# Kernel tuning notes

Hardware: AMD Instinct MI355X
Metric: run time of the kernel (lower is better)

The kernel has to match this reference:

```python
import jax, jax.numpy as jnp
import numpy as np

D_MODEL = 1024
N_HEADS = 16
HEAD_DIM = D_MODEL // N_HEADS


def setup_inputs() -> dict:
    key = jax.random.key(0)
    ks = jax.random.split(key, 9)
    B, S, D = 2, 2048, D_MODEL
    scale = 1.0 / np.sqrt(D)
    return {
        "q": jax.random.normal(ks[0], (B, S, D), jnp.float32),
        "k": jax.random.normal(ks[1], (B, S, D), jnp.float32),
        "v": jax.random.normal(ks[2], (B, S, D), jnp.float32),
        "Wq": jax.random.normal(ks[3], (D, D), jnp.float32) * scale,
        "bq": jax.random.normal(ks[4], (D,), jnp.float32) * 0.01,
        "Wk": jax.random.normal(ks[5], (D, D), jnp.float32) * scale,
        "bk": jax.random.normal(ks[6], (D,), jnp.float32) * 0.01,
        "Wv": jax.random.normal(ks[7], (D, D), jnp.float32) * scale,
        "bv": jax.random.normal(ks[8], (D,), jnp.float32) * 0.01,
    }


def reference(q, k, v, Wq, bq, Wk, bk, Wv, bv):
    B, S, D = q.shape
    H, Dh = N_HEADS, D // N_HEADS
    # linear projections (torch Linear: x @ W.T + b)
    qp = q @ Wq.T + bq
    kp = k @ Wk.T + bk
    vp = v @ Wv.T + bv
    # [B, S, H, Dh] -> [B, H, S, Dh]
    qh = qp.reshape(B, S, H, Dh).transpose(0, 2, 1, 3)
    kh = kp.reshape(B, S, H, Dh).transpose(0, 2, 1, 3)
    vh = vp.reshape(B, S, H, Dh).transpose(0, 2, 1, 3)
    # scaled dot-product attention (mask=None path)
    scores = jnp.einsum('bhqd,bhkd->bhqk', qh, kh) / jnp.sqrt(jnp.asarray(Dh, qh.dtype))
    attn = jax.nn.softmax(scores, axis=-1)
    out = jnp.einsum('bhqk,bhkd->bhqd', attn, vh)
    # [B, H, S, Dh] -> [B, S, D]
    return out.transpose(0, 2, 1, 3).reshape(B, S, D)
```

## Files before the change

kernel.cpp:

```cpp
#include <hip/hip_runtime.h>
#include <stdint.h>
#include <stddef.h>


#define NH  16
#define DH  64
#define SEQ 2048
#define DM  1024
#define NB  2

#define ACT_N (NB * SEQ * DM)
#define W_N   (DM * DM)
#define QSCALE 0.18033688011116012f

typedef float  f32x4  __attribute__((ext_vector_type(4)));
typedef __bf16 bf16x8 __attribute__((ext_vector_type(8)));
typedef __bf16 bf16x4 __attribute__((ext_vector_type(4)));

__device__ __forceinline__ __bf16 f2bf(float f) { return (__bf16)f; }

__device__ __forceinline__ float fexp2(float x) {
    float r; asm("v_exp_f32 %0, %1" : "=v"(r) : "v"(x)); return r;
}

__device__ __forceinline__ void gload_lds16(const void* g, void* l) {
    __builtin_amdgcn_global_load_lds(
        (const __attribute__((address_space(1))) void*)g,
        (__attribute__((address_space(3))) void*)l, 16, 0, 0);
}

__global__ __launch_bounds__(256) void cvt6(
    const float* __restrict__ s0, const float* __restrict__ s1,
    const float* __restrict__ s2, const float* __restrict__ s3,
    const float* __restrict__ s4, const float* __restrict__ s5,
    __bf16* __restrict__ d0, __bf16* __restrict__ d1, __bf16* __restrict__ d2,
    __bf16* __restrict__ d3, __bf16* __restrict__ d4, __bf16* __restrict__ d5)
{
    const float* s; __bf16* d; int n;
    switch (blockIdx.z) {
        case 0: s = s0; d = d0; n = ACT_N; break;
        case 1: s = s1; d = d1; n = ACT_N; break;
        case 2: s = s2; d = d2; n = ACT_N; break;
        case 3: s = s3; d = d3; n = W_N;   break;
        case 4: s = s4; d = d4; n = W_N;   break;
        default: s = s5; d = d5; n = W_N;  break;
    }
    const size_t i = ((size_t)blockIdx.x * 256 + threadIdx.x) * 8;
    if (i >= (size_t)n) return;
    float4 f0 = *(const float4*)(s + i);
    float4 f1 = *(const float4*)(s + i + 4);
    bf16x8 o;
    o[0] = f2bf(f0.x); o[1] = f2bf(f0.y); o[2] = f2bf(f0.z); o[3] = f2bf(f0.w);
    o[4] = f2bf(f1.x); o[5] = f2bf(f1.y); o[6] = f2bf(f1.z); o[7] = f2bf(f1.w);
    *(bf16x8*)(d + i) = o;
}

__global__ __launch_bounds__(512) void proj3(
    const __bf16* __restrict__ Xq, const __bf16* __restrict__ Xk, const __bf16* __restrict__ Xv,
    const __bf16* __restrict__ Wq, const __bf16* __restrict__ Wk, const __bf16* __restrict__ Wv,
    const float* __restrict__ bq, const float* __restrict__ bk, const float* __restrict__ bv,
    __bf16* __restrict__ dq, __bf16* __restrict__ dk, __bf16* __restrict__ dv)
{
    __shared__ __align__(16) __bf16 sA[2][16384];
    __shared__ __align__(16) __bf16 sB[2][16384];

    const int tid  = threadIdx.x;
    const int lane = tid & 63;
    const int wv   = tid >> 6;
    const int wm   = wv >> 2;
    const int wn   = wv & 3;
    const int tensor = blockIdx.y >> 2;
    const int nb   = (blockIdx.y & 3) * 256;
    const int mb   = blockIdx.x * 256;

    const __bf16 *X, *W; const float* bias; __bf16* dst;
    if (tensor == 0)      { X = Xq; W = Wq; bias = bq; dst = dq; }
    else if (tensor == 1) { X = Xk; W = Wk; bias = bk; dst = dk; }
    else                  { X = Xv; W = Wv; bias = bv; dst = dv; }
    const bool vpath = (tensor == 2);

    const int lr = lane & 15;
    const int lg = lane >> 4;

    const int srow = lane >> 3;
    const int gch  = (lane & 7) ^ srow;
    const __bf16* xs = X + (size_t)(mb + wv * 32 + srow) * DM + gch * 8;
    const __bf16* ws = W + (size_t)(nb + wv * 32 + srow) * DM + gch * 8;

#define LA(BUF, T, I) gload_lds16(xs + (size_t)(T) * 64 + (size_t)(I) * 8 * DM, \
                                  &sA[BUF][(wv * 32 + (I) * 8) * 64])
#define LB(BUF, T, I) gload_lds16(ws + (size_t)(T) * 64 + (size_t)(I) * 8 * DM, \
                                  &sB[BUF][(wv * 32 + (I) * 8) * 64])

    const int rsw = (lr & 7) << 4;
    const int rdk0 = (0 * 64 + lg * 16) ^ rsw;
    const int rdk1 = (1 * 64 + lg * 16) ^ rsw;
    const int arow = (wm * 128 + lr) * 128;
    const int brow = (wn * 64 + lr) * 128;

    f32x4 acc[32];
#pragma unroll
    for (int i = 0; i < 32; ++i) acc[i] = (f32x4){0.f, 0.f, 0.f, 0.f};

    bf16x8 aP[4], aQ2[4], bP[4], bQ2[4];

#define RDA(R, CA, MH, KS) { \
    _Pragma("unroll") for (int mt = 0; mt < 4; ++mt) \
        R[mt] = *(const bf16x8*)((CA) + arow + ((MH) * 4 + mt) * 16 * 128 + ((KS) ? rdk1 : rdk0)); }
#define RDB(R, CB, KS) { \
    _Pragma("unroll") for (int nt = 0; nt < 4; ++nt) \
        R[nt] = *(const bf16x8*)((CB) + brow + nt * 16 * 128 + ((KS) ? rdk1 : rdk0)); }

#define MFMAQ(MH, AA, BB) { \
    __builtin_amdgcn_s_setprio(1); \
    if (!vpath) { \
        _Pragma("unroll") for (int nt = 0; nt < 4; ++nt) \
        _Pragma("unroll") for (int mt = 0; mt < 4; ++mt) \
            acc[nt * 8 + (MH) * 4 + mt] = __builtin_amdgcn_mfma_f32_16x16x32_bf16( \
                BB[nt], AA[mt], acc[nt * 8 + (MH) * 4 + mt], 0, 0, 0); \
    } else { \
        _Pragma("unroll") for (int mt = 0; mt < 4; ++mt) \
        _Pragma("unroll") for (int nt = 0; nt < 4; ++nt) \
            acc[((MH) * 4 + mt) * 4 + nt] = __builtin_amdgcn_mfma_f32_16x16x32_bf16( \
                AA[mt], BB[nt], acc[((MH) * 4 + mt) * 4 + nt], 0, 0, 0); } \
    __builtin_amdgcn_s_setprio(0); }

#pragma unroll
    for (int i = 0; i < 4; ++i) { LA(0, 0, i); LB(0, 0, i); }
    __syncthreads();
    {
        const char* ca = (const char*)&sA[0][0];
        const char* cb = (const char*)&sB[0][0];
        RDA(aP, ca, 0, 0);
        RDB(bP, cb, 0);
    }

#pragma unroll
    for (int t = 0; t < 16; ++t) {
        const int cur = t & 1, nxt = cur ^ 1;
        const char* ca = (const char*)&sA[cur][0];
        const char* cb = (const char*)&sB[cur][0];
        const char* caN = (const char*)&sA[nxt][0];
        const char* cbN = (const char*)&sB[nxt][0];
        const bool more = (t + 1 < 16);

        if (more) { LA(nxt, t + 1, 0); LA(nxt, t + 1, 1); LB(nxt, t + 1, 0); }
        RDA(aQ2, ca, 1, 0);
        MFMAQ(0, aP, bP);

        if (more) { LA(nxt, t + 1, 2); LA(nxt, t + 1, 3); LB(nxt, t + 1, 1); }
        RDA(aP, ca, 0, 1);
        RDB(bQ2, cb, 1);
        MFMAQ(1, aQ2, bP);

        if (more) { LB(nxt, t + 1, 2); LB(nxt, t + 1, 3); }
        RDA(aQ2, ca, 1, 1);
        MFMAQ(0, aP, bQ2);

        MFMAQ(1, aQ2, bQ2);
        if (more) {
            __syncthreads();
            RDA(aP, caN, 0, 0);
            RDB(bP, cbN, 0);
        }
    }
#undef MFMAQ
#undef RDA
#undef RDB
#undef LA
#undef LB

    if (!vpath) {
        const float scale = (tensor == 0) ? QSCALE : 1.0f;
#pragma unroll
        for (int nt = 0; nt < 4; ++nt) {
            const int n_base = nb + wn * 64 + nt * 16 + lg * 4;
            const float4 bb = *(const float4*)&bias[n_base];
            const int h = n_base >> 6, dh = n_base & 63;
#pragma unroll
            for (int mt = 0; mt < 8; ++mt) {
                const int m_g = mb + wm * 128 + mt * 16 + lr;
                const int bi = m_g >> 11;
                const int s  = m_g & (SEQ - 1);
                const f32x4 v = acc[nt * 8 + mt];
                bf16x4 w;
                w[0] = f2bf((v[0] + bb.x) * scale);
                w[1] = f2bf((v[1] + bb.y) * scale);
                w[2] = f2bf((v[2] + bb.z) * scale);
                w[3] = f2bf((v[3] + bb.w) * scale);
                *(bf16x4*)&dst[((size_t)((bi * NH + h) * SEQ + s)) * DH + dh] = w;
            }
        }
    } else {
        const int h = (nb + wn * 64) >> 6;
#pragma unroll
        for (int nt = 0; nt < 4; ++nt) {
            const int n_g = nb + wn * 64 + nt * 16 + lr;
            const float bb = bias[n_g];
            const int dh = n_g & 63;
#pragma unroll
            for (int mt = 0; mt < 8; ++mt) {
                const int m_g = mb + wm * 128 + mt * 16 + lg * 4;
                const int bi = m_g >> 11;
                const int s0 = m_g & (SEQ - 1);
                const f32x4 v = acc[mt * 4 + nt];
                bf16x4 w;
#pragma unroll
                for (int r = 0; r < 4; ++r) w[r] = f2bf(v[r] + bb);
                *(bf16x4*)&dst[((size_t)((bi * NH + h) * DH + dh)) * SEQ + s0] = w;
            }
        }
    }
}

__global__ __launch_bounds__(256) void attn_kernel(
    const __bf16* __restrict__ qh, const __bf16* __restrict__ kh,
    const __bf16* __restrict__ vT, float* __restrict__ out)
{
    __shared__ __align__(16) __bf16 kbuf[3][4096];
    __shared__ __align__(16) __bf16 vbuf[3][4096];

    const int tid  = threadIdx.x;
    const int lane = tid & 63;
    const int wv   = tid >> 6;
    const int i    = blockIdx.x;
    const int slot = i >> 3;
    const int bh   = (i & 7) * 4 + (slot >> 4);
    const int qt   = slot & 15;
    const size_t hb = (size_t)bh * SEQ * DH;
    const int q0 = qt * 128 + wv * 32;
    const int lq = lane & 15;
    const int lg = lane >> 4;
    const int swz = (lq & 7) << 4;

    const int p0 = tid, p1 = tid + 256;
    const int c0 = (p0 ^ ((p0 >> 3) & 7)) & 7;
    const int c1 = (p1 ^ ((p1 >> 3) & 7)) & 7;
    const int r0 = p0 >> 3, r1 = p1 >> 3;
    const int gr0 = (r0 & 35) | ((r0 & 12) << 1) | ((r0 & 16) >> 2);
    const int gr1 = (r1 & 35) | ((r1 & 12) << 1) | ((r1 & 16) >> 2);
    const __bf16* ks0 = kh + hb + (size_t)gr0 * DH + c0 * 8;
    const __bf16* ks1 = kh + hb + (size_t)gr1 * DH + c1 * 8;
    const __bf16* vs0 = vT + hb + (size_t)r0 * SEQ + c0 * 8;
    const __bf16* vs1 = vT + hb + (size_t)r1 * SEQ + c1 * 8;
    const int dst0 = wv * 512;
    const int dst1 = 2048 + wv * 512;

#define STAGE(SEL, TI) { \
    gload_lds16(ks0 + (size_t)(TI) * 64 * DH, &kbuf[SEL][dst0]); \
    gload_lds16(ks1 + (size_t)(TI) * 64 * DH, &kbuf[SEL][dst1]); \
    gload_lds16(vs0 + (TI) * 64, &vbuf[SEL][dst0]); \
    gload_lds16(vs1 + (TI) * 64, &vbuf[SEL][dst1]); }

    bf16x8 bQ[2][2];
#pragma unroll
    for (int qtf = 0; qtf < 2; ++qtf)
#pragma unroll
        for (int ks = 0; ks < 2; ++ks)
            bQ[qtf][ks] = *(const bf16x8*)(qh + hb +
                (size_t)(q0 + qtf * 16 + lq) * DH + ks * 32 + lg * 8);

    bf16x8 ONES;
#pragma unroll
    for (int e = 0; e < 8; ++e) ONES[e] = f2bf(1.0f);

    f32x4 O[2][4];
#pragma unroll
    for (int qtf = 0; qtf < 2; ++qtf)
#pragma unroll
        for (int dt = 0; dt < 4; ++dt) O[qtf][dt] = (f32x4){0.f, 0.f, 0.f, 0.f};
    f32x4 Ol[2];
    Ol[0] = (f32x4){0.f, 0.f, 0.f, 0.f};
    Ol[1] = (f32x4){0.f, 0.f, 0.f, 0.f};

    const int rdk0 = lq * 128 + ((0 * 64 + lg * 16) ^ swz);
    const int rdk1 = lq * 128 + ((1 * 64 + lg * 16) ^ swz);

    f32x4 scA[2][4], scB[2][4];
    bf16x8 paf[2][2];

#define QK(SL, SC) { \
    const char* kc = (const char*)&kbuf[SL][0]; \
    _Pragma("unroll") for (int kt = 0; kt < 4; ++kt) { \
        const bf16x8 ak0 = *(const bf16x8*)(kc + kt * 2048 + rdk0); \
        const bf16x8 ak1 = *(const bf16x8*)(kc + kt * 2048 + rdk1); \
        _Pragma("unroll") for (int qtf = 0; qtf < 2; ++qtf) { \
            f32x4 c = (f32x4){0.f, 0.f, 0.f, 0.f}; \
            c = __builtin_amdgcn_mfma_f32_16x16x32_bf16(ak0, bQ[qtf][0], c, 0, 0, 0); \
            c = __builtin_amdgcn_mfma_f32_16x16x32_bf16(ak1, bQ[qtf][1], c, 0, 0, 0); \
            SC[qtf][kt] = c; } } }

#define SMAX(SC) { \
    _Pragma("unroll") for (int qtf = 0; qtf < 2; ++qtf) \
    _Pragma("unroll") for (int ks = 0; ks < 2; ++ks) { \
        bf16x8 w; \
        _Pragma("unroll") for (int r = 0; r < 4; ++r) { \
            w[r]     = f2bf(fexp2(SC[qtf][2 * ks][r])); \
            w[4 + r] = f2bf(fexp2(SC[qtf][2 * ks + 1][r])); } \
        paf[qtf][ks] = w; } }

#define PV(SL) { \
    const char* vc = (const char*)&vbuf[SL][0]; \
    _Pragma("unroll") for (int ks = 0; ks < 2; ++ks) { \
        const int rd = (ks == 0) ? rdk0 : rdk1; \
        _Pragma("unroll") for (int dt = 0; dt < 4; ++dt) { \
            const bf16x8 bv = *(const bf16x8*)(vc + dt * 2048 + rd); \
            O[0][dt] = __builtin_amdgcn_mfma_f32_16x16x32_bf16(paf[0][ks], bv, O[0][dt], 0, 0, 0); \
            O[1][dt] = __builtin_amdgcn_mfma_f32_16x16x32_bf16(paf[1][ks], bv, O[1][dt], 0, 0, 0); } \
        Ol[0] = __builtin_amdgcn_mfma_f32_16x16x32_bf16(paf[0][ks], ONES, Ol[0], 0, 0, 0); \
        Ol[1] = __builtin_amdgcn_mfma_f32_16x16x32_bf16(paf[1][ks], ONES, Ol[1], 0, 0, 0); } }

#define BODY(T, SCUR, SNXT) { \
    SMAX(SCUR); \
    __syncthreads(); \
    if ((T) + 2 < 32) STAGE(((T) + 2) % 3, (T) + 2); \
    __builtin_amdgcn_s_setprio(1); \
    if ((T) + 1 < 32) QK(((T) + 1) % 3, SNXT); \
    PV((T) % 3); \
    __builtin_amdgcn_s_setprio(0); }

    STAGE(0, 0);
    STAGE(1, 1);
    __syncthreads();
    QK(0, scA);

#pragma unroll
    for (int t = 0; t < 32; t += 2) {
        BODY(t, scA, scB);
        BODY(t + 1, scB, scA);
    }
#undef BODY
#undef PV
#undef SMAX
#undef QK
#undef STAGE

    const int b = bh >> 4, h = bh & 15;
#pragma unroll
    for (int qtf = 0; qtf < 2; ++qtf) {
#pragma unroll
        for (int r = 0; r < 4; ++r) {
            const float li = 1.0f / (qtf ? Ol[1][r] : Ol[0][r]);
            const int s_g = q0 + qtf * 16 + lg * 4 + r;
            float* op = out + ((size_t)(b * SEQ + s_g)) * DM + h * DH;
#pragma unroll
            for (int dt = 0; dt < 4; ++dt)
                op[dt * 16 + lq] = O[qtf][dt][r] * li;
        }
    }
}

extern "C" void kernel_launch(void* const* d_in, const int* in_sizes, int n_in,
                              void* d_out, int out_size, void* d_ws, size_t ws_size,
                              hipStream_t stream)
{
    (void)in_sizes; (void)n_in; (void)out_size; (void)ws_size;
    const float* q  = (const float*)d_in[0];
    const float* k  = (const float*)d_in[1];
    const float* v  = (const float*)d_in[2];
    const float* Wq = (const float*)d_in[3];
    const float* bq = (const float*)d_in[4];
    const float* Wk = (const float*)d_in[5];
    const float* bk = (const float*)d_in[6];
    const float* Wv = (const float*)d_in[7];
    const float* bv = (const float*)d_in[8];

    const size_t act = (size_t)ACT_N;
    const size_t wn  = (size_t)W_N;
    __bf16* qx  = (__bf16*)d_ws;
    __bf16* kx  = qx + act;
    __bf16* vx  = kx + act;
    __bf16* wqb = vx + act;
    __bf16* wkb = wqb + wn;
    __bf16* wvb = wkb + wn;
    __bf16* qhd = wvb + wn;
    __bf16* khd = qhd + act;
    __bf16* vhd = khd + act;
    float* out = (float*)d_out;

    cvt6<<<dim3(2048, 1, 6), dim3(256), 0, stream>>>(
        q, k, v, Wq, Wk, Wv, qx, kx, vx, wqb, wkb, wvb);
    proj3<<<dim3(16, 12), dim3(512), 0, stream>>>(
        qx, kx, vx, wqb, wkb, wvb, bq, bk, bv, qhd, khd, vhd);
    attn_kernel<<<dim3(512), dim3(256), 0, stream>>>(qhd, khd, vhd, out);
}
```

Measured before the change: 90.09 us.

## Shrink projection GEMM tiles to 128x128 with XCD-aware block remapping

The fused QKV projection now uses 128x128 output tiles computed by 256-thread blocks instead of 256x256 tiles with 512 threads, which raises the grid from 192 to 768 blocks so all compute units are filled. A linear block index is remapped so that consecutive tiles land on the same XCD group, aiming for better L2 reuse of X and W rows. Each warp's accumulators and the LDS footprint shrink, but every block gets less data reuse per tile and makes more global loads for the same work.

```diff
diff --git a/kernel.cpp b/kernel.cpp
--- a/kernel.cpp
+++ b/kernel.cpp
@@ -55,23 +55,21 @@
     *(bf16x8*)(d + i) = o;
 }
 
-__global__ __launch_bounds__(512) void proj3(
+__global__ __launch_bounds__(256) void proj3(
     const __bf16* __restrict__ Xq, const __bf16* __restrict__ Xk, const __bf16* __restrict__ Xv,
     const __bf16* __restrict__ Wq, const __bf16* __restrict__ Wk, const __bf16* __restrict__ Wv,
     const float* __restrict__ bq, const float* __restrict__ bk, const float* __restrict__ bv,
     __bf16* __restrict__ dq, __bf16* __restrict__ dk, __bf16* __restrict__ dv)
 {
-    __shared__ __align__(16) __bf16 sA[2][16384];
-    __shared__ __align__(16) __bf16 sB[2][16384];
-
-    const int tid  = threadIdx.x;
-    const int lane = tid & 63;
-    const int wv   = tid >> 6;
-    const int wm   = wv >> 2;
-    const int wn   = wv & 3;
-    const int tensor = blockIdx.y >> 2;
-    const int nb   = (blockIdx.y & 3) * 256;
-    const int mb   = blockIdx.x * 256;
+    __shared__ __align__(16) __bf16 sA[2][8192];
+    __shared__ __align__(16) __bf16 sB[2][8192];
+
+    const int li   = blockIdx.x;
+    const int j    = (li & 7) * 96 + (li >> 3);
+    const int mb   = (j / 24) * 128;
+    const int nbg  = (j % 24) * 128;
+    const int tensor = nbg >> 10;
+    const int nb   = nbg & 1023;
 
     const __bf16 *X, *W; const float* bias; __bf16* dst;
     if (tensor == 0)      { X = Xq; W = Wq; bias = bq; dst = dq; }
@@ -79,6 +77,10 @@
     else                  { X = Xv; W = Wv; bias = bv; dst = dv; }
     const bool vpath = (tensor == 2);
 
+    const int lane = threadIdx.x & 63;
+    const int wv   = threadIdx.x >> 6;
+    const int lm0  = (wv >> 1) * 64;
+    const int ln0  = (wv & 1) * 64;
     const int lr = lane & 15;
     const int lg = lane >> 4;
 
@@ -92,37 +94,37 @@
 #define LB(BUF, T, I) gload_lds16(ws + (size_t)(T) * 64 + (size_t)(I) * 8 * DM, \
                                   &sB[BUF][(wv * 32 + (I) * 8) * 64])
 
-    const int rsw = (lr & 7) << 4;
+    const int rsw  = (lr & 7) << 4;
     const int rdk0 = (0 * 64 + lg * 16) ^ rsw;
     const int rdk1 = (1 * 64 + lg * 16) ^ rsw;
-    const int arow = (wm * 128 + lr) * 128;
-    const int brow = (wn * 64 + lr) * 128;
-
-    f32x4 acc[32];
-#pragma unroll
-    for (int i = 0; i < 32; ++i) acc[i] = (f32x4){0.f, 0.f, 0.f, 0.f};
-
-    bf16x8 aP[4], aQ2[4], bP[4], bQ2[4];
-
-#define RDA(R, CA, MH, KS) { \
+    const int arow = (lm0 + lr) * 128;
+    const int brow = (ln0 + lr) * 128;
+
+    f32x4 acc[16];
+#pragma unroll
+    for (int i = 0; i < 16; ++i) acc[i] = (f32x4){0.f, 0.f, 0.f, 0.f};
+
+    bf16x8 aP[4], bP[4], aQ2[4], bQ2[4];
+
+#define RDA(R, CA, KS) { \
     _Pragma("unroll") for (int mt = 0; mt < 4; ++mt) \
-        R[mt] = *(const bf16x8*)((CA) + arow + ((MH) * 4 + mt) * 16 * 128 + ((KS) ? rdk1 : rdk0)); }
+        R[mt] = *(const bf16x8*)((CA) + arow + mt * 16 * 128 + ((KS) ? rdk1 : rdk0)); }
 #define RDB(R, CB, KS) { \
     _Pragma("unroll") for (int nt = 0; nt < 4; ++nt) \
         R[nt] = *(const bf16x8*)((CB) + brow + nt * 16 * 128 + ((KS) ? rdk1 : rdk0)); }
 
-#define MFMAQ(MH, AA, BB) { \
+#define MFMAQ(AA, BB) { \
     __builtin_amdgcn_s_setprio(1); \
     if (!vpath) { \
         _Pragma("unroll") for (int nt = 0; nt < 4; ++nt) \
         _Pragma("unroll") for (int mt = 0; mt < 4; ++mt) \
-            acc[nt * 8 + (MH) * 4 + mt] = __builtin_amdgcn_mfma_f32_16x16x32_bf16( \
-                BB[nt], AA[mt], acc[nt * 8 + (MH) * 4 + mt], 0, 0, 0); \
+            acc[nt * 4 + mt] = __builtin_amdgcn_mfma_f32_16x16x32_bf16( \
+                BB[nt], AA[mt], acc[nt * 4 + mt], 0, 0, 0); \
     } else { \
         _Pragma("unroll") for (int mt = 0; mt < 4; ++mt) \
         _Pragma("unroll") for (int nt = 0; nt < 4; ++nt) \
-            acc[((MH) * 4 + mt) * 4 + nt] = __builtin_amdgcn_mfma_f32_16x16x32_bf16( \
-                AA[mt], BB[nt], acc[((MH) * 4 + mt) * 4 + nt], 0, 0, 0); } \
+            acc[mt * 4 + nt] = __builtin_amdgcn_mfma_f32_16x16x32_bf16( \
+                AA[mt], BB[nt], acc[mt * 4 + nt], 0, 0, 0); } \
     __builtin_amdgcn_s_setprio(0); }
 
 #pragma unroll
@@ -131,36 +133,29 @@
     {
         const char* ca = (const char*)&sA[0][0];
         const char* cb = (const char*)&sB[0][0];
-        RDA(aP, ca, 0, 0);
+        RDA(aP, ca, 0);
         RDB(bP, cb, 0);
     }
 
 #pragma unroll
     for (int t = 0; t < 16; ++t) {
         const int cur = t & 1, nxt = cur ^ 1;
-        const char* ca = (const char*)&sA[cur][0];
-        const char* cb = (const char*)&sB[cur][0];
+        const char* ca  = (const char*)&sA[cur][0];
+        const char* cb  = (const char*)&sB[cur][0];
         const char* caN = (const char*)&sA[nxt][0];
         const char* cbN = (const char*)&sB[nxt][0];
         const bool more = (t + 1 < 16);
 
-        if (more) { LA(nxt, t + 1, 0); LA(nxt, t + 1, 1); LB(nxt, t + 1, 0); }
-        RDA(aQ2, ca, 1, 0);
-        MFMAQ(0, aP, bP);
-
-        if (more) { LA(nxt, t + 1, 2); LA(nxt, t + 1, 3); LB(nxt, t + 1, 1); }
-        RDA(aP, ca, 0, 1);
+        if (more) { LA(nxt, t + 1, 0); LA(nxt, t + 1, 1); LB(nxt, t + 1, 0); LB(nxt, t + 1, 1); }
+        RDA(aQ2, ca, 1);
         RDB(bQ2, cb, 1);
-        MFMAQ(1, aQ2, bP);
-
-        if (more) { LB(nxt, t + 1, 2); LB(nxt, t + 1, 3); }
-        RDA(aQ2, ca, 1, 1);
-        MFMAQ(0, aP, bQ2);
-
-        MFMAQ(1, aQ2, bQ2);
+        MFMAQ(aP, bP);
+
+        if (more) { LA(nxt, t + 1, 2); LA(nxt, t + 1, 3); LB(nxt, t + 1, 2); LB(nxt, t + 1, 3); }
+        MFMAQ(aQ2, bQ2);
         if (more) {
             __syncthreads();
-            RDA(aP, caN, 0, 0);
+            RDA(aP, caN, 0);
             RDB(bP, cbN, 0);
         }
     }
@@ -174,15 +169,15 @@
         const float scale = (tensor == 0) ? QSCALE : 1.0f;
 #pragma unroll
         for (int nt = 0; nt < 4; ++nt) {
-            const int n_base = nb + wn * 64 + nt * 16 + lg * 4;
+            const int n_base = nb + ln0 + nt * 16 + lg * 4;
             const float4 bb = *(const float4*)&bias[n_base];
             const int h = n_base >> 6, dh = n_base & 63;
 #pragma unroll
-            for (int mt = 0; mt < 8; ++mt) {
-                const int m_g = mb + wm * 128 + mt * 16 + lr;
+            for (int mt = 0; mt < 4; ++mt) {
+                const int m_g = mb + lm0 + mt * 16 + lr;
                 const int bi = m_g >> 11;
                 const int s  = m_g & (SEQ - 1);
-                const f32x4 v = acc[nt * 8 + mt];
+                const f32x4 v = acc[nt * 4 + mt];
                 bf16x4 w;
                 w[0] = f2bf((v[0] + bb.x) * scale);
                 w[1] = f2bf((v[1] + bb.y) * scale);
@@ -192,15 +187,15 @@
             }
         }
     } else {
-        const int h = (nb + wn * 64) >> 6;
+        const int h = (nb + ln0) >> 6;
 #pragma unroll
         for (int nt = 0; nt < 4; ++nt) {
-            const int n_g = nb + wn * 64 + nt * 16 + lr;
+            const int n_g = nb + ln0 + nt * 16 + lr;
             const float bb = bias[n_g];
             const int dh = n_g & 63;
 #pragma unroll
-            for (int mt = 0; mt < 8; ++mt) {
-                const int m_g = mb + wm * 128 + mt * 16 + lg * 4;
+            for (int mt = 0; mt < 4; ++mt) {
+                const int m_g = mb + lm0 + mt * 16 + lg * 4;
                 const int bi = m_g >> 11;
                 const int s0 = m_g & (SEQ - 1);
                 const f32x4 v = acc[mt * 4 + nt];
@@ -380,7 +375,7 @@
 
     cvt6<<<dim3(2048, 1, 6), dim3(256), 0, stream>>>(
         q, k, v, Wq, Wk, Wv, qx, kx, vx, wqb, wkb, wvb);
-    proj3<<<dim3(16, 12), dim3(512), 0, stream>>>(
+    proj3<<<dim3(768), dim3(256), 0, stream>>>(
         qx, kx, vx, wqb, wkb, wvb, bq, bk, bv, qhd, khd, vhd);
     attn_kernel<<<dim3(512), dim3(256), 0, stream>>>(qhd, khd, vhd, out);
 }
```

Result: slower. 111.2 us (+23.4%).
